# Kernel tuning notes

Hardware: AMD Instinct MI355X
Metric: run time of the kernel (lower is better)

Reference implementation:

```python
import jax, jax.numpy as jnp
import numpy as np

# Graph sizes: users -> items ('ui') and users -> tags ('ut'), plus reverse etypes.
N_U, N_I, N_T, D = 100000, 50000, 20000, 128
E_UI, E_UT = 500000, 300000


def setup_inputs() -> dict:
    key = jax.random.key(0)
    k = jax.random.split(key, 7)
    return {
        "h_u": jax.random.normal(k[0], (N_U, D), jnp.float32),
        "h_i": jax.random.normal(k[1], (N_I, D), jnp.float32),
        "h_t": jax.random.normal(k[2], (N_T, D), jnp.float32),
        "ui_src": jax.random.randint(k[3], (E_UI,), 0, N_U, jnp.int32),
        "ui_dst": jax.random.randint(k[4], (E_UI,), 0, N_I, jnp.int32),
        "ut_src": jax.random.randint(k[5], (E_UT,), 0, N_U, jnp.int32),
        "ut_dst": jax.random.randint(k[6], (E_UT,), 0, N_T, jnp.int32),
    }


def _seg_sum(x, idx, n):
    return jax.ops.segment_sum(x, idx, num_segments=n)


def _deg(idx, n):
    # in-degree, clamped to min 1 (as torch .clamp(min=1))
    return jnp.clip(_seg_sum(jnp.ones(idx.shape, jnp.float32), idx, n), 1.0, None)


def reference(h_u, h_i, h_t, ui_src, ui_dst, ut_src, ut_dst):
    NORM_2 = -1.0  # default norm_2 arg
    # forward pass: copy_u('h') + sum per etype, then 1/in_degree normalization on dst
    rst_i = _seg_sum(h_u[ui_src], ui_dst, N_I) / _deg(ui_dst, N_I)[:, None]  # [N_I, D]
    rst_t = _seg_sum(h_u[ut_src], ut_dst, N_T) / _deg(ut_dst, N_T)[:, None]  # [N_T, D]
    # backward pass: multi_update_all over reverse etypes, 'sum' cross-etype reducer
    bsrc = _seg_sum(rst_i[ui_dst], ui_src, N_U) + _seg_sum(rst_t[ut_dst], ut_src, N_U)
    # in_degrees_b: per-etype clamped degrees summed across reverse etypes
    deg_b = _deg(ui_src, N_U) + _deg(ut_src, N_U)
    bsrc = bsrc * (deg_b ** NORM_2)[:, None]
    # rst is the LAST etype's normalized dst result ('ut' -> tags)
    return bsrc, rst_t
```

## Files before the change

### kernel.cpp

```cpp
#include <hip/hip_runtime.h>

#define NU 100000
#define NI 50000
#define NT 20000
#define DD 128
#define EUI 500000
#define EUT 300000

#define B_I   0
#define B_T   (NI)
#define B_UUI (NI + NT)
#define B_UUT (NI + NT + NU)
#define NSCAN (NI + NT + NU + NU)
#define TOTAL_E (2 * (EUI + EUT))

#define BPB   512
#define NB    ((NSCAN + BPB - 1) / BPB)
#define CH    8192
#define NBLK  ((TOTAL_E + CH - 1) / CH)
#define NHIST (NB * NBLK)

__device__ __forceinline__ unsigned bfpack(float a, float b) {
    unsigned ua = __float_as_uint(a), ub = __float_as_uint(b);
    ua = (ua + 0x7FFFu + ((ua >> 16) & 1u)) >> 16;
    ub = (ub + 0x7FFFu + ((ub >> 16) & 1u)) >> 16;
    return ua | (ub << 16);
}
__device__ __forceinline__ void bacc(unsigned p, float& a, float& b) {
    a += __uint_as_float(p << 16);
    b += __uint_as_float(p & 0xFFFF0000u);
}

__device__ __forceinline__ void entry_of(int e,
        const int* __restrict__ ui_src, const int* __restrict__ ui_dst,
        const int* __restrict__ ut_src, const int* __restrict__ ut_dst,
        int& bucket, int& val) {
    if (e < EUI)              { bucket = B_I   + ui_dst[e];              val = ui_src[e]; }
    else if (e < 2 * EUI)     { int j = e - EUI;       bucket = B_UUI + ui_src[j]; val = ui_dst[j]; }
    else if (e < 2 * EUI + EUT){ int j = e - 2 * EUI;   bucket = B_T   + ut_dst[j]; val = ut_src[j]; }
    else                      { int j = e - 2 * EUI - EUT; bucket = B_UUT + ut_src[j]; val = ut_dst[j]; }
}


__global__ void k_hist(const int* __restrict__ ui_src, const int* __restrict__ ui_dst,
                       const int* __restrict__ ut_src, const int* __restrict__ ut_dst,
                       int* __restrict__ hist) {
    __shared__ int h[NB];
    int b = blockIdx.x, t = threadIdx.x;
    for (int i = t; i < NB; i += 256) h[i] = 0;
    __syncthreads();
    int e0 = b * CH;
    int e1 = min(e0 + CH, TOTAL_E);
    for (int e = e0 + t; e < e1; e += 256) {
        int bucket, val;
        entry_of(e, ui_src, ui_dst, ut_src, ut_dst, bucket, val);
        (void)val;
        atomicAdd(&h[bucket >> 9], 1);
    }
    __syncthreads();
    for (int i = t; i < NB; i += 256) hist[i * NBLK + b] = h[i];
}

__global__ void k_scanA(int* __restrict__ data, int* __restrict__ bsums, int n) {
    __shared__ int lds[256];
    int b = blockIdx.x, t = threadIdx.x;
    int base = b * 1024 + t * 4;
    int v0 = (base + 0 < n) ? data[base + 0] : 0;
    int v1 = (base + 1 < n) ? data[base + 1] : 0;
    int v2 = (base + 2 < n) ? data[base + 2] : 0;
    int v3 = (base + 3 < n) ? data[base + 3] : 0;
    int i0 = v0, i1 = i0 + v1, i2 = i1 + v2, i3 = i2 + v3;
    lds[t] = i3;
    __syncthreads();
    for (int o = 1; o < 256; o <<= 1) {
        int x = (t >= o) ? lds[t - o] : 0;
        __syncthreads();
        lds[t] += x;
        __syncthreads();
    }
    int ex = lds[t] - i3;
    if (base + 0 < n) data[base + 0] = ex + i0;
    if (base + 1 < n) data[base + 1] = ex + i1;
    if (base + 2 < n) data[base + 2] = ex + i2;
    if (base + 3 < n) data[base + 3] = ex + i3;
    if (t == 255) bsums[b] = lds[255];
}

__global__ void k_scanB(int* __restrict__ bsums, int nsb) {
    __shared__ int lds[512];
    int t = threadIdx.x;
    int a = (t < nsb) ? bsums[t] : 0;
    int b2 = (t + 256 < nsb) ? bsums[t + 256] : 0;
    lds[t] = a;
    lds[t + 256] = b2;
    __syncthreads();
    for (int o = 1; o < 512; o <<= 1) {
        int x0 = (t >= o) ? lds[t - o] : 0;
        int x1 = (t + 256 >= o) ? lds[t + 256 - o] : 0;
        __syncthreads();
        lds[t] += x0;
        lds[t + 256] += x1;
        __syncthreads();
    }
    if (t < nsb) bsums[t] = lds[t] - a;
    if (t + 256 < nsb) bsums[t + 256] = lds[t + 256] - b2;
}

__global__ void k_scanC(int* __restrict__ data, const int* __restrict__ bsums, int n) {
    int b = blockIdx.x;
    int add = bsums[b];
    int base = b * 1024 + threadIdx.x * 4;
    if (base + 0 < n) data[base + 0] += add;
    if (base + 1 < n) data[base + 1] += add;
    if (base + 2 < n) data[base + 2] += add;
    if (base + 3 < n) data[base + 3] += add;
}

__global__ void k_scatterbin(const int* __restrict__ ui_src, const int* __restrict__ ui_dst,
                             const int* __restrict__ ut_src, const int* __restrict__ ut_dst,
                             const int* __restrict__ hist, unsigned* __restrict__ binned) {
    __shared__ int loff[NB];
    int b = blockIdx.x, t = threadIdx.x;
    for (int i = t; i < NB; i += 256) loff[i] = hist[i * NBLK + b];
    __syncthreads();
    int e0 = b * CH;
    int e1 = min(e0 + CH, TOTAL_E);
    for (int e = e0 + t; e < e1; e += 256) {
        int bucket, val;
        entry_of(e, ui_src, ui_dst, ut_src, ut_dst, bucket, val);
        int bin = bucket >> 9;
        int pos = atomicAdd(&loff[bin], -1) - 1;
        binned[pos] = ((unsigned)(bucket & (BPB - 1)) << 17) | (unsigned)val;
    }
}


__global__ void k_bincount(const unsigned* __restrict__ binned,
                           const int* __restrict__ hist, int* __restrict__ off) {
    __shared__ int cnt[BPB];
    int b = blockIdx.x, t = threadIdx.x;
    cnt[t] = 0; cnt[t + 256] = 0;
    __syncthreads();
    int s = (b == 0) ? 0 : hist[b * NBLK - 1];
    int e = hist[(b + 1) * NBLK - 1];
    for (int i = s + t; i < e; i += 256) atomicAdd(&cnt[binned[i] >> 17], 1);
    __syncthreads();
    int base = b * BPB;
    if (base + t < NSCAN) off[base + t] = cnt[t];
    if (base + t + 256 < NSCAN) off[base + t + 256] = cnt[t + 256];
}

__global__ void k_finescatter(const unsigned* __restrict__ binned,
                              const int* __restrict__ hist,
                              int* __restrict__ off, int* __restrict__ edges) {
    __shared__ int loff[BPB];
    int b = blockIdx.x, t = threadIdx.x;
    int base = b * BPB;
    if (base + t < NSCAN) loff[t] = off[base + t];
    if (base + t + 256 < NSCAN) loff[t + 256] = off[base + t + 256];
    __syncthreads();
    int s = (b == 0) ? 0 : hist[b * NBLK - 1];
    int e = hist[(b + 1) * NBLK - 1];
    for (int i = s + t; i < e; i += 256) {
        unsigned v = binned[i];
        int local = v >> 17;
        int pos = atomicAdd(&loff[local], -1) - 1;
        edges[pos] = (int)(v & 0x1FFFFu);
    }
    __syncthreads();
    if (base + t < NSCAN) off[base + t] = loff[t];
    if (base + t + 256 < NSCAN) off[base + t + 256] = loff[t + 256];
}

__global__ void k_cvt(const float4* __restrict__ in, uint4* __restrict__ out) {
    int t = blockIdx.x * blockDim.x + threadIdx.x;
    if (t >= NU * DD / 8) return;
    float4 a = in[t * 2 + 0];
    float4 b = in[t * 2 + 1];
    uint4 o;
    o.x = bfpack(a.x, a.y); o.y = bfpack(a.z, a.w);
    o.z = bfpack(b.x, b.y); o.w = bfpack(b.z, b.w);
    out[t] = o;
}

__global__ void k_gather_fwd_b(const uint2* __restrict__ feat,
                               const int* __restrict__ off, const int* __restrict__ edges,
                               uint2* __restrict__ outb, float4* __restrict__ outf,
                               int base, int nrows) {
    int tid = blockIdx.x * blockDim.x + threadIdx.x;
    int r = tid >> 5;
    int c = tid & 31;
    if (r >= nrows) return;
    int g = base + r;
    int start = off[g];
    int end = (g + 1 < NSCAN) ? off[g + 1] : TOTAL_E;
    float a0 = 0.f, a1 = 0.f, a2 = 0.f, a3 = 0.f;
    float b0 = 0.f, b1 = 0.f, b2 = 0.f, b3 = 0.f;
    int e = start;
    for (; e + 2 <= end; e += 2) {
        int s0 = edges[e], s1 = edges[e + 1];
        uint2 p0 = feat[(size_t)s0 * 32 + c];
        uint2 p1 = feat[(size_t)s1 * 32 + c];
        bacc(p0.x, a0, a1); bacc(p0.y, a2, a3);
        bacc(p1.x, b0, b1); bacc(p1.y, b2, b3);
    }
    if (e < end) {
        uint2 p = feat[(size_t)edges[e] * 32 + c];
        bacc(p.x, a0, a1); bacc(p.y, a2, a3);
    }
    float inv = 1.0f / fmaxf((float)(end - start), 1.0f);
    a0 = (a0 + b0) * inv; a1 = (a1 + b1) * inv;
    a2 = (a2 + b2) * inv; a3 = (a3 + b3) * inv;
    uint2 ob; ob.x = bfpack(a0, a1); ob.y = bfpack(a2, a3);
    outb[(size_t)r * 32 + c] = ob;
    if (outf) {
        float4 of; of.x = a0; of.y = a1; of.z = a2; of.w = a3;
        outf[(size_t)r * 32 + c] = of;
    }
}

__global__ void k_gather_fwd_f(const float4* __restrict__ feat,
                               const int* __restrict__ off, const int* __restrict__ edges,
                               uint2* __restrict__ outb, float4* __restrict__ outf,
                               int base, int nrows) {
    int tid = blockIdx.x * blockDim.x + threadIdx.x;
    int r = tid >> 5;
    int c = tid & 31;
    if (r >= nrows) return;
    int g = base + r;
    int start = off[g];
    int end = (g + 1 < NSCAN) ? off[g + 1] : TOTAL_E;
    float a0 = 0.f, a1 = 0.f, a2 = 0.f, a3 = 0.f;
    float b0 = 0.f, b1 = 0.f, b2 = 0.f, b3 = 0.f;
    int e = start;
    for (; e + 2 <= end; e += 2) {
        int s0 = edges[e], s1 = edges[e + 1];
        float4 v0 = feat[(size_t)s0 * 32 + c];
        float4 v1 = feat[(size_t)s1 * 32 + c];
        a0 += v0.x; a1 += v0.y; a2 += v0.z; a3 += v0.w;
        b0 += v1.x; b1 += v1.y; b2 += v1.z; b3 += v1.w;
    }
    if (e < end) {
        float4 v = feat[(size_t)edges[e] * 32 + c];
        a0 += v.x; a1 += v.y; a2 += v.z; a3 += v.w;
    }
    float inv = 1.0f / fmaxf((float)(end - start), 1.0f);
    a0 = (a0 + b0) * inv; a1 = (a1 + b1) * inv;
    a2 = (a2 + b2) * inv; a3 = (a3 + b3) * inv;
    uint2 ob; ob.x = bfpack(a0, a1); ob.y = bfpack(a2, a3);
    outb[(size_t)r * 32 + c] = ob;
    if (outf) {
        float4 of; of.x = a0; of.y = a1; of.z = a2; of.w = a3;
        outf[(size_t)r * 32 + c] = of;
    }
}

__global__ void k_gather_bwd_b(const uint2* __restrict__ rst_i,
                               const uint2* __restrict__ rst_t,
                               const int* __restrict__ off, const int* __restrict__ edges,
                               float4* __restrict__ bsrc) {
    int tid = blockIdx.x * blockDim.x + threadIdx.x;
    int r = tid >> 5;
    int c = tid & 31;
    if (r >= NU) return;
    int g1 = B_UUI + r;
    int s1 = off[g1], e1 = off[g1 + 1];
    int g2 = B_UUT + r;
    int s2 = off[g2], e2 = (g2 + 1 < NSCAN) ? off[g2 + 1] : TOTAL_E;
    float a0 = 0.f, a1 = 0.f, a2 = 0.f, a3 = 0.f;
    float b0 = 0.f, b1 = 0.f, b2 = 0.f, b3 = 0.f;
    int e = s1;
    for (; e + 2 <= e1; e += 2) {
        int d0 = edges[e], d1 = edges[e + 1];
        uint2 p0 = rst_i[(size_t)d0 * 32 + c];
        uint2 p1 = rst_i[(size_t)d1 * 32 + c];
        bacc(p0.x, a0, a1); bacc(p0.y, a2, a3);
        bacc(p1.x, b0, b1); bacc(p1.y, b2, b3);
    }
    if (e < e1) {
        uint2 p = rst_i[(size_t)edges[e] * 32 + c];
        bacc(p.x, a0, a1); bacc(p.y, a2, a3);
    }
    e = s2;
    for (; e + 2 <= e2; e += 2) {
        int d0 = edges[e], d1 = edges[e + 1];
        uint2 p0 = rst_t[(size_t)d0 * 32 + c];
        uint2 p1 = rst_t[(size_t)d1 * 32 + c];
        bacc(p0.x, a0, a1); bacc(p0.y, a2, a3);
        bacc(p1.x, b0, b1); bacc(p1.y, b2, b3);
    }
    if (e < e2) {
        uint2 p = rst_t[(size_t)edges[e] * 32 + c];
        bacc(p.x, a0, a1); bacc(p.y, a2, a3);
    }
    float inv = 1.0f / (fmaxf((float)(e1 - s1), 1.0f) + fmaxf((float)(e2 - s2), 1.0f));
    float4 o;
    o.x = (a0 + b0) * inv; o.y = (a1 + b1) * inv;
    o.z = (a2 + b2) * inv; o.w = (a3 + b3) * inv;
    bsrc[(size_t)r * 32 + c] = o;
}

__global__ void k_count_old(const int4* __restrict__ ui_src, const int4* __restrict__ ui_dst,
                            const int4* __restrict__ ut_src, const int4* __restrict__ ut_dst,
                            int* __restrict__ off) {
    int i = blockIdx.x * blockDim.x + threadIdx.x;
    if (i < EUI / 4) {
        int4 s = ui_src[i], d = ui_dst[i];
        atomicAdd(&off[B_I + d.x], 1); atomicAdd(&off[B_I + d.y], 1);
        atomicAdd(&off[B_I + d.z], 1); atomicAdd(&off[B_I + d.w], 1);
        atomicAdd(&off[B_UUI + s.x], 1); atomicAdd(&off[B_UUI + s.y], 1);
        atomicAdd(&off[B_UUI + s.z], 1); atomicAdd(&off[B_UUI + s.w], 1);
    } else if (i < EUI / 4 + EUT / 4) {
        int j = i - EUI / 4;
        int4 s = ut_src[j], d = ut_dst[j];
        atomicAdd(&off[B_T + d.x], 1); atomicAdd(&off[B_T + d.y], 1);
        atomicAdd(&off[B_T + d.z], 1); atomicAdd(&off[B_T + d.w], 1);
        atomicAdd(&off[B_UUT + s.x], 1); atomicAdd(&off[B_UUT + s.y], 1);
        atomicAdd(&off[B_UUT + s.z], 1); atomicAdd(&off[B_UUT + s.w], 1);
    }
}

__global__ void k_fill_old(const int2* __restrict__ ui_src, const int2* __restrict__ ui_dst,
                           const int2* __restrict__ ut_src, const int2* __restrict__ ut_dst,
                           int* __restrict__ off, int* __restrict__ edges) {
    int i = blockIdx.x * blockDim.x + threadIdx.x;
    if (i < EUI / 2) {
        int2 s = ui_src[i], d = ui_dst[i];
        edges[atomicAdd(&off[B_I + d.x], -1) - 1] = s.x;
        edges[atomicAdd(&off[B_UUI + s.x], -1) - 1] = d.x;
        edges[atomicAdd(&off[B_I + d.y], -1) - 1] = s.y;
        edges[atomicAdd(&off[B_UUI + s.y], -1) - 1] = d.y;
    } else if (i < EUI / 2 + EUT / 2) {
        int j = i - EUI / 2;
        int2 s = ut_src[j], d = ut_dst[j];
        edges[atomicAdd(&off[B_T + d.x], -1) - 1] = s.x;
        edges[atomicAdd(&off[B_UUT + s.x], -1) - 1] = d.x;
        edges[atomicAdd(&off[B_T + d.y], -1) - 1] = s.y;
        edges[atomicAdd(&off[B_UUT + s.y], -1) - 1] = d.y;
    }
}

__global__ void f_count(const int* __restrict__ ui_src, const int* __restrict__ ui_dst,
                        const int* __restrict__ ut_src, const int* __restrict__ ut_dst,
                        float* __restrict__ cnt_uui, float* __restrict__ cnt_i,
                        float* __restrict__ cnt_uut, float* __restrict__ cnt_t) {
    int i = blockIdx.x * blockDim.x + threadIdx.x;
    if (i < EUI) {
        unsafeAtomicAdd(&cnt_uui[ui_src[i]], 1.0f);
        unsafeAtomicAdd(&cnt_i[ui_dst[i]], 1.0f);
    } else if (i < EUI + EUT) {
        int j = i - EUI;
        unsafeAtomicAdd(&cnt_uut[ut_src[j]], 1.0f);
        unsafeAtomicAdd(&cnt_t[ut_dst[j]], 1.0f);
    }
}
__global__ void f_scatter_fwd(const float4* __restrict__ feat, const int* __restrict__ src,
                              const int* __restrict__ dst, float* __restrict__ out_sum, int nedge) {
    int tid = blockIdx.x * blockDim.x + threadIdx.x;
    int e = tid >> 5, c = tid & 31;
    if (e >= nedge) return;
    float4 v = feat[(size_t)src[e] * 32 + c];
    float* o = out_sum + (size_t)dst[e] * DD + c * 4;
    unsafeAtomicAdd(o + 0, v.x); unsafeAtomicAdd(o + 1, v.y);
    unsafeAtomicAdd(o + 2, v.z); unsafeAtomicAdd(o + 3, v.w);
}
__global__ void f_scatter_bwd(const float4* __restrict__ rst_sum, const float* __restrict__ cnt,
                              const int* __restrict__ src, const int* __restrict__ dst,
                              float* __restrict__ bsrc, int nedge) {
    int tid = blockIdx.x * blockDim.x + threadIdx.x;
    int e = tid >> 5, c = tid & 31;
    if (e >= nedge) return;
    float inv = 1.0f / fmaxf(cnt[dst[e]], 1.0f);
    float4 v = rst_sum[(size_t)dst[e] * 32 + c];
    float* o = bsrc + (size_t)src[e] * DD + c * 4;
    unsafeAtomicAdd(o + 0, v.x * inv); unsafeAtomicAdd(o + 1, v.y * inv);
    unsafeAtomicAdd(o + 2, v.z * inv); unsafeAtomicAdd(o + 3, v.w * inv);
}
__global__ void f_norm(float4* __restrict__ rst, const float* __restrict__ cnt, int nrows) {
    int tid = blockIdx.x * blockDim.x + threadIdx.x;
    int r = tid >> 5, c = tid & 31;
    if (r >= nrows) return;
    float inv = 1.0f / fmaxf(cnt[r], 1.0f);
    float4 v = rst[(size_t)r * 32 + c];
    v.x *= inv; v.y *= inv; v.z *= inv; v.w *= inv;
    rst[(size_t)r * 32 + c] = v;
}
__global__ void f_final(float4* __restrict__ bsrc, const float* __restrict__ cnt_a,
                        const float* __restrict__ cnt_b, int nrows) {
    int tid = blockIdx.x * blockDim.x + threadIdx.x;
    int r = tid >> 5, c = tid & 31;
    if (r >= nrows) return;
    float inv = 1.0f / (fmaxf(cnt_a[r], 1.0f) + fmaxf(cnt_b[r], 1.0f));
    float4 v = bsrc[(size_t)r * 32 + c];
    v.x *= inv; v.y *= inv; v.z *= inv; v.w *= inv;
    bsrc[(size_t)r * 32 + c] = v;
}


extern "C" void kernel_launch(void* const* d_in, const int* in_sizes, int n_in,
                              void* d_out, int out_size, void* d_ws, size_t ws_size,
                              hipStream_t stream) {
    const float* h_u  = (const float*)d_in[0];
    const int* ui_src = (const int*)d_in[3];
    const int* ui_dst = (const int*)d_in[4];
    const int* ut_src = (const int*)d_in[5];
    const int* ut_dst = (const int*)d_in[6];

    float* bsrc  = (float*)d_out;
    float* rst_t = (float*)d_out + (size_t)NU * DD;

    const int B = 256;

    const size_t INT_WORDS = (size_t)NSCAN + 512 + TOTAL_E;
    const size_t BASE_B    = INT_WORDS * 4;
    const size_t HUB_B     = (size_t)NU * DD * 2;
    const size_t RIB_B     = (size_t)NI * DD * 2;
    const size_t RTB_B     = (size_t)NT * DD * 2;
    const size_t NEED_FULL = BASE_B + HUB_B + RIB_B + RTB_B;
    const size_t NEED_HALF = BASE_B + RIB_B + RTB_B;

    if (ws_size >= NEED_FULL) {
        int* off      = (int*)d_ws;
        int* bsums    = off + NSCAN;
        int* edges    = bsums + 512;
        uint2* hu_b   = (uint2*)((char*)d_ws + BASE_B);
        uint2* rsti_b = (uint2*)((char*)d_ws + BASE_B + HUB_B);
        uint2* rstt_b = (uint2*)((char*)d_ws + BASE_B + HUB_B + RIB_B);
        unsigned* binned = (unsigned*)rsti_b;
        int* hist        = (int*)rstt_b;

        k_cvt<<<(NU * DD / 8 + B - 1) / B, B, 0, stream>>>(
            (const float4*)h_u, (uint4*)hu_b);

        k_hist<<<NBLK, B, 0, stream>>>(ui_src, ui_dst, ut_src, ut_dst, hist);

        {
            int nblk = (NHIST + 1023) / 1024;
            k_scanA<<<nblk, B, 0, stream>>>(hist, bsums, NHIST);
            k_scanB<<<1, B, 0, stream>>>(bsums, nblk);
            k_scanC<<<nblk, B, 0, stream>>>(hist, bsums, NHIST);
        }

        k_scatterbin<<<NBLK, B, 0, stream>>>(ui_src, ui_dst, ut_src, ut_dst, hist, binned);

        k_bincount<<<NB, B, 0, stream>>>(binned, hist, off);

        {
            int nblk = (NSCAN + 1023) / 1024;
            k_scanA<<<nblk, B, 0, stream>>>(off, bsums, NSCAN);
            k_scanB<<<1, B, 0, stream>>>(bsums, nblk);
            k_scanC<<<nblk, B, 0, stream>>>(off, bsums, NSCAN);
        }

        k_finescatter<<<NB, B, 0, stream>>>(binned, hist, off, edges);

        k_gather_fwd_b<<<((long)NI * 32 + B - 1) / B, B, 0, stream>>>(
            hu_b, off, edges, rsti_b, (float4*)nullptr, B_I, NI);
        k_gather_fwd_b<<<((long)NT * 32 + B - 1) / B, B, 0, stream>>>(
            hu_b, off, edges, rstt_b, (float4*)rst_t, B_T, NT);
        k_gather_bwd_b<<<((long)NU * 32 + B - 1) / B, B, 0, stream>>>(
            rsti_b, rstt_b, off, edges, (float4*)bsrc);
    } else if (ws_size >= NEED_HALF) {
        int* off   = (int*)d_ws;
        int* bsums = off + NSCAN;
        int* edges = bsums + 512;
        uint2* rsti_b = (uint2*)((char*)d_ws + BASE_B);
        uint2* rstt_b = (uint2*)((char*)d_ws + BASE_B + RIB_B);

        hipMemsetAsync(off, 0, (NSCAN + 512) * sizeof(int), stream);

        int nq = EUI / 4 + EUT / 4;
        k_count_old<<<(nq + B - 1) / B, B, 0, stream>>>(
            (const int4*)ui_src, (const int4*)ui_dst,
            (const int4*)ut_src, (const int4*)ut_dst, off);
        {
            int nblk = (NSCAN + 1023) / 1024;
            k_scanA<<<nblk, B, 0, stream>>>(off, bsums, NSCAN);
            k_scanB<<<1, B, 0, stream>>>(bsums, nblk);
            k_scanC<<<nblk, B, 0, stream>>>(off, bsums, NSCAN);
        }
        int nh = EUI / 2 + EUT / 2;
        k_fill_old<<<(nh + B - 1) / B, B, 0, stream>>>(
            (const int2*)ui_src, (const int2*)ui_dst,
            (const int2*)ut_src, (const int2*)ut_dst, off, edges);

        k_gather_fwd_f<<<((long)NI * 32 + B - 1) / B, B, 0, stream>>>(
            (const float4*)h_u, off, edges, rsti_b, (float4*)nullptr, B_I, NI);
        k_gather_fwd_f<<<((long)NT * 32 + B - 1) / B, B, 0, stream>>>(
            (const float4*)h_u, off, edges, rstt_b, (float4*)rst_t, B_T, NT);
        k_gather_bwd_b<<<((long)NU * 32 + B - 1) / B, B, 0, stream>>>(
            rsti_b, rstt_b, off, edges, (float4*)bsrc);
    } else {
        float* ws        = (float*)d_ws;
        float* rst_i_sum = ws;
        float* cnt_i     = rst_i_sum + (size_t)NI * DD;
        float* cnt_t     = cnt_i + NI;
        float* cnt_uui   = cnt_t + NT;
        float* cnt_uut   = cnt_uui + NU;
        size_t ws_floats = (size_t)NI * DD + NI + NT + NU + NU;

        hipMemsetAsync(d_ws, 0, ws_floats * sizeof(float), stream);
        hipMemsetAsync(d_out, 0, (size_t)out_size * sizeof(float), stream);

        int n = EUI + EUT;
        f_count<<<(n + B - 1) / B, B, 0, stream>>>(ui_src, ui_dst, ut_src, ut_dst,
                                                   cnt_uui, cnt_i, cnt_uut, cnt_t);
        f_scatter_fwd<<<((long)EUI * 32 + B - 1) / B, B, 0, stream>>>(
            (const float4*)h_u, ui_src, ui_dst, rst_i_sum, EUI);
        f_scatter_fwd<<<((long)EUT * 32 + B - 1) / B, B, 0, stream>>>(
            (const float4*)h_u, ut_src, ut_dst, rst_t, EUT);
        f_scatter_bwd<<<((long)EUI * 32 + B - 1) / B, B, 0, stream>>>(
            (const float4*)rst_i_sum, cnt_i, ui_src, ui_dst, bsrc, EUI);
        f_scatter_bwd<<<((long)EUT * 32 + B - 1) / B, B, 0, stream>>>(
            (const float4*)rst_t, cnt_t, ut_src, ut_dst, bsrc, EUT);
        f_norm<<<((long)NT * 32 + B - 1) / B, B, 0, stream>>>((float4*)rst_t, cnt_t, NT);
        f_final<<<((long)NU * 32 + B - 1) / B, B, 0, stream>>>((float4*)bsrc, cnt_uui, cnt_uut, NU);
    }
}
```

Before: 194.5 us.

## Merge forward gathers and use 16-lane rows with uint4 loads and shuffled indices

Replaces the two forward gather launches with one kernel covering item and tag rows, since their CSR offsets are contiguous. Both forward and backward gathers now assign 16 lanes per row, with each lane loading 8 bf16 values as a uint4. Each lane loads one edge index per batch of 16, and the index is broadcast with a width-16 shuffle instead of every lane reading it. The aim is fewer launches, wider memory transactions and less index traffic. The cost is the loss of the dual-accumulator unrolling and more register pressure per thread. The old 32-lane kernels are kept, simplified, for the fallback path.

```diff
diff --git a/kernel.cpp b/kernel.cpp
--- a/kernel.cpp
+++ b/kernel.cpp
@@ -40,7 +40,6 @@
     else if (e < 2 * EUI + EUT){ int j = e - 2 * EUI;   bucket = B_T   + ut_dst[j]; val = ut_src[j]; }
     else                      { int j = e - 2 * EUI - EUT; bucket = B_UUT + ut_src[j]; val = ut_dst[j]; }
 }
-
 
 __global__ void k_hist(const int* __restrict__ ui_src, const int* __restrict__ ui_dst,
                        const int* __restrict__ ut_src, const int* __restrict__ ut_dst,
@@ -134,7 +133,6 @@
     }
 }
 
-
 __global__ void k_bincount(const unsigned* __restrict__ binned,
                            const int* __restrict__ hist, int* __restrict__ off) {
     __shared__ int cnt[BPB];
@@ -183,121 +181,84 @@
     out[t] = o;
 }
 
-__global__ void k_gather_fwd_b(const uint2* __restrict__ feat,
-                               const int* __restrict__ off, const int* __restrict__ edges,
-                               uint2* __restrict__ outb, float4* __restrict__ outf,
-                               int base, int nrows) {
-    int tid = blockIdx.x * blockDim.x + threadIdx.x;
-    int r = tid >> 5;
-    int c = tid & 31;
-    if (r >= nrows) return;
-    int g = base + r;
-    int start = off[g];
-    int end = (g + 1 < NSCAN) ? off[g + 1] : TOTAL_E;
-    float a0 = 0.f, a1 = 0.f, a2 = 0.f, a3 = 0.f;
-    float b0 = 0.f, b1 = 0.f, b2 = 0.f, b3 = 0.f;
-    int e = start;
-    for (; e + 2 <= end; e += 2) {
-        int s0 = edges[e], s1 = edges[e + 1];
-        uint2 p0 = feat[(size_t)s0 * 32 + c];
-        uint2 p1 = feat[(size_t)s1 * 32 + c];
-        bacc(p0.x, a0, a1); bacc(p0.y, a2, a3);
-        bacc(p1.x, b0, b1); bacc(p1.y, b2, b3);
-    }
-    if (e < end) {
-        uint2 p = feat[(size_t)edges[e] * 32 + c];
-        bacc(p.x, a0, a1); bacc(p.y, a2, a3);
+
+__global__ void g_fwd(const uint4* __restrict__ feat,
+                      const int* __restrict__ off, const int* __restrict__ edges,
+                      uint4* __restrict__ rsti_b, uint4* __restrict__ rstt_b,
+                      float4* __restrict__ outf) {
+    int tid = blockIdx.x * blockDim.x + threadIdx.x;
+    int r = tid >> 4;
+    int c = tid & 15;
+    if (r >= NI + NT) return;
+    int start = off[r];
+    int end = off[r + 1];
+    float a0=0.f,a1=0.f,a2=0.f,a3=0.f,a4=0.f,a5=0.f,a6=0.f,a7=0.f;
+    for (int base = start; base < end; base += 16) {
+        int n = min(16, end - base);
+        int eidx = (c < n) ? edges[base + c] : 0;
+        #pragma unroll 4
+        for (int k = 0; k < n; ++k) {
+            int s = __shfl(eidx, k, 16);
+            uint4 p = feat[(size_t)s * 16 + c];
+            bacc(p.x, a0, a1); bacc(p.y, a2, a3);
+            bacc(p.z, a4, a5); bacc(p.w, a6, a7);
+        }
     }
     float inv = 1.0f / fmaxf((float)(end - start), 1.0f);
-    a0 = (a0 + b0) * inv; a1 = (a1 + b1) * inv;
-    a2 = (a2 + b2) * inv; a3 = (a3 + b3) * inv;
-    uint2 ob; ob.x = bfpack(a0, a1); ob.y = bfpack(a2, a3);
-    outb[(size_t)r * 32 + c] = ob;
-    if (outf) {
-        float4 of; of.x = a0; of.y = a1; of.z = a2; of.w = a3;
-        outf[(size_t)r * 32 + c] = of;
-    }
-}
-
-__global__ void k_gather_fwd_f(const float4* __restrict__ feat,
-                               const int* __restrict__ off, const int* __restrict__ edges,
-                               uint2* __restrict__ outb, float4* __restrict__ outf,
-                               int base, int nrows) {
-    int tid = blockIdx.x * blockDim.x + threadIdx.x;
-    int r = tid >> 5;
-    int c = tid & 31;
-    if (r >= nrows) return;
-    int g = base + r;
-    int start = off[g];
-    int end = (g + 1 < NSCAN) ? off[g + 1] : TOTAL_E;
-    float a0 = 0.f, a1 = 0.f, a2 = 0.f, a3 = 0.f;
-    float b0 = 0.f, b1 = 0.f, b2 = 0.f, b3 = 0.f;
-    int e = start;
-    for (; e + 2 <= end; e += 2) {
-        int s0 = edges[e], s1 = edges[e + 1];
-        float4 v0 = feat[(size_t)s0 * 32 + c];
-        float4 v1 = feat[(size_t)s1 * 32 + c];
-        a0 += v0.x; a1 += v0.y; a2 += v0.z; a3 += v0.w;
-        b0 += v1.x; b1 += v1.y; b2 += v1.z; b3 += v1.w;
-    }
-    if (e < end) {
-        float4 v = feat[(size_t)edges[e] * 32 + c];
-        a0 += v.x; a1 += v.y; a2 += v.z; a3 += v.w;
-    }
-    float inv = 1.0f / fmaxf((float)(end - start), 1.0f);
-    a0 = (a0 + b0) * inv; a1 = (a1 + b1) * inv;
-    a2 = (a2 + b2) * inv; a3 = (a3 + b3) * inv;
-    uint2 ob; ob.x = bfpack(a0, a1); ob.y = bfpack(a2, a3);
-    outb[(size_t)r * 32 + c] = ob;
-    if (outf) {
-        float4 of; of.x = a0; of.y = a1; of.z = a2; of.w = a3;
-        outf[(size_t)r * 32 + c] = of;
-    }
-}
-
-__global__ void k_gather_bwd_b(const uint2* __restrict__ rst_i,
-                               const uint2* __restrict__ rst_t,
-                               const int* __restrict__ off, const int* __restrict__ edges,
-                               float4* __restrict__ bsrc) {
-    int tid = blockIdx.x * blockDim.x + threadIdx.x;
-    int r = tid >> 5;
-    int c = tid & 31;
+    a0*=inv; a1*=inv; a2*=inv; a3*=inv; a4*=inv; a5*=inv; a6*=inv; a7*=inv;
+    uint4 ob;
+    ob.x = bfpack(a0,a1); ob.y = bfpack(a2,a3);
+    ob.z = bfpack(a4,a5); ob.w = bfpack(a6,a7);
+    if (r < NI) {
+        rsti_b[(size_t)r * 16 + c] = ob;
+    } else {
+        int rt = r - NI;
+        rstt_b[(size_t)rt * 16 + c] = ob;
+        float4 f0; f0.x=a0; f0.y=a1; f0.z=a2; f0.w=a3;
+        float4 f1; f1.x=a4; f1.y=a5; f1.z=a6; f1.w=a7;
+        outf[(size_t)rt * 32 + c*2 + 0] = f0;
+        outf[(size_t)rt * 32 + c*2 + 1] = f1;
+    }
+}
+
+__global__ void g_bwd(const uint4* __restrict__ rst_i, const uint4* __restrict__ rst_t,
+                      const int* __restrict__ off, const int* __restrict__ edges,
+                      float4* __restrict__ bsrc) {
+    int tid = blockIdx.x * blockDim.x + threadIdx.x;
+    int r = tid >> 4;
+    int c = tid & 15;
     if (r >= NU) return;
-    int g1 = B_UUI + r;
-    int s1 = off[g1], e1 = off[g1 + 1];
+    int s1 = off[B_UUI + r], e1 = off[B_UUI + r + 1];
     int g2 = B_UUT + r;
     int s2 = off[g2], e2 = (g2 + 1 < NSCAN) ? off[g2 + 1] : TOTAL_E;
-    float a0 = 0.f, a1 = 0.f, a2 = 0.f, a3 = 0.f;
-    float b0 = 0.f, b1 = 0.f, b2 = 0.f, b3 = 0.f;
-    int e = s1;
-    for (; e + 2 <= e1; e += 2) {
-        int d0 = edges[e], d1 = edges[e + 1];
-        uint2 p0 = rst_i[(size_t)d0 * 32 + c];
-        uint2 p1 = rst_i[(size_t)d1 * 32 + c];
-        bacc(p0.x, a0, a1); bacc(p0.y, a2, a3);
-        bacc(p1.x, b0, b1); bacc(p1.y, b2, b3);
-    }
-    if (e < e1) {
-        uint2 p = rst_i[(size_t)edges[e] * 32 + c];
-        bacc(p.x, a0, a1); bacc(p.y, a2, a3);
-    }
-    e = s2;
-    for (; e + 2 <= e2; e += 2) {
-        int d0 = edges[e], d1 = edges[e + 1];
-        uint2 p0 = rst_t[(size_t)d0 * 32 + c];
-        uint2 p1 = rst_t[(size_t)d1 * 32 + c];
-        bacc(p0.x, a0, a1); bacc(p0.y, a2, a3);
-        bacc(p1.x, b0, b1); bacc(p1.y, b2, b3);
-    }
-    if (e < e2) {
-        uint2 p = rst_t[(size_t)edges[e] * 32 + c];
-        bacc(p.x, a0, a1); bacc(p.y, a2, a3);
+    float a0=0.f,a1=0.f,a2=0.f,a3=0.f,a4=0.f,a5=0.f,a6=0.f,a7=0.f;
+    for (int base = s1; base < e1; base += 16) {
+        int n = min(16, e1 - base);
+        int eidx = (c < n) ? edges[base + c] : 0;
+        #pragma unroll 4
+        for (int k = 0; k < n; ++k) {
+            int d = __shfl(eidx, k, 16);
+            uint4 p = rst_i[(size_t)d * 16 + c];
+            bacc(p.x, a0, a1); bacc(p.y, a2, a3);
+            bacc(p.z, a4, a5); bacc(p.w, a6, a7);
+        }
+    }
+    for (int base = s2; base < e2; base += 16) {
+        int n = min(16, e2 - base);
+        int eidx = (c < n) ? edges[base + c] : 0;
+        #pragma unroll 4
+        for (int k = 0; k < n; ++k) {
+            int d = __shfl(eidx, k, 16);
+            uint4 p = rst_t[(size_t)d * 16 + c];
+            bacc(p.x, a0, a1); bacc(p.y, a2, a3);
+            bacc(p.z, a4, a5); bacc(p.w, a6, a7);
+        }
     }
     float inv = 1.0f / (fmaxf((float)(e1 - s1), 1.0f) + fmaxf((float)(e2 - s2), 1.0f));
-    float4 o;
-    o.x = (a0 + b0) * inv; o.y = (a1 + b1) * inv;
-    o.z = (a2 + b2) * inv; o.w = (a3 + b3) * inv;
-    bsrc[(size_t)r * 32 + c] = o;
+    float4 f0; f0.x=a0*inv; f0.y=a1*inv; f0.z=a2*inv; f0.w=a3*inv;
+    float4 f1; f1.x=a4*inv; f1.y=a5*inv; f1.z=a6*inv; f1.w=a7*inv;
+    bsrc[(size_t)r * 32 + c*2 + 0] = f0;
+    bsrc[(size_t)r * 32 + c*2 + 1] = f1;
 }
 
 __global__ void k_count_old(const int4* __restrict__ ui_src, const int4* __restrict__ ui_dst,
@@ -340,6 +301,59 @@
     }
 }
 
+__global__ void k_gather_fwd_f(const float4* __restrict__ feat,
+                               const int* __restrict__ off, const int* __restrict__ edges,
+                               uint2* __restrict__ outb, float4* __restrict__ outf,
+                               int base, int nrows) {
+    int tid = blockIdx.x * blockDim.x + threadIdx.x;
+    int r = tid >> 5;
+    int c = tid & 31;
+    if (r >= nrows) return;
+    int g = base + r;
+    int start = off[g];
+    int end = (g + 1 < NSCAN) ? off[g + 1] : TOTAL_E;
+    float a0 = 0.f, a1 = 0.f, a2 = 0.f, a3 = 0.f;
+    for (int e = start; e < end; ++e) {
+        float4 v = feat[(size_t)edges[e] * 32 + c];
+        a0 += v.x; a1 += v.y; a2 += v.z; a3 += v.w;
+    }
+    float inv = 1.0f / fmaxf((float)(end - start), 1.0f);
+    a0 *= inv; a1 *= inv; a2 *= inv; a3 *= inv;
+    uint2 ob; ob.x = bfpack(a0, a1); ob.y = bfpack(a2, a3);
+    outb[(size_t)r * 32 + c] = ob;
+    if (outf) {
+        float4 of; of.x = a0; of.y = a1; of.z = a2; of.w = a3;
+        outf[(size_t)r * 32 + c] = of;
+    }
+}
+
+__global__ void k_gather_bwd_b(const uint2* __restrict__ rst_i,
+                               const uint2* __restrict__ rst_t,
+                               const int* __restrict__ off, const int* __restrict__ edges,
+                               float4* __restrict__ bsrc) {
+    int tid = blockIdx.x * blockDim.x + threadIdx.x;
+    int r = tid >> 5;
+    int c = tid & 31;
+    if (r >= NU) return;
+    int g1 = B_UUI + r;
+    int s1 = off[g1], e1 = off[g1 + 1];
+    int g2 = B_UUT + r;
+    int s2 = off[g2], e2 = (g2 + 1 < NSCAN) ? off[g2 + 1] : TOTAL_E;
+    float a0 = 0.f, a1 = 0.f, a2 = 0.f, a3 = 0.f;
+    for (int e = s1; e < e1; ++e) {
+        uint2 p = rst_i[(size_t)edges[e] * 32 + c];
+        bacc(p.x, a0, a1); bacc(p.y, a2, a3);
+    }
+    for (int e = s2; e < e2; ++e) {
+        uint2 p = rst_t[(size_t)edges[e] * 32 + c];
+        bacc(p.x, a0, a1); bacc(p.y, a2, a3);
+    }
+    float inv = 1.0f / (fmaxf((float)(e1 - s1), 1.0f) + fmaxf((float)(e2 - s2), 1.0f));
+    float4 o;
+    o.x = a0 * inv; o.y = a1 * inv; o.z = a2 * inv; o.w = a3 * inv;
+    bsrc[(size_t)r * 32 + c] = o;
+}
+
 __global__ void f_count(const int* __restrict__ ui_src, const int* __restrict__ ui_dst,
                         const int* __restrict__ ut_src, const int* __restrict__ ut_dst,
                         float* __restrict__ cnt_uui, float* __restrict__ cnt_i,
@@ -423,14 +437,14 @@
         int* off      = (int*)d_ws;
         int* bsums    = off + NSCAN;
         int* edges    = bsums + 512;
-        uint2* hu_b   = (uint2*)((char*)d_ws + BASE_B);
-        uint2* rsti_b = (uint2*)((char*)d_ws + BASE_B + HUB_B);
-        uint2* rstt_b = (uint2*)((char*)d_ws + BASE_B + HUB_B + RIB_B);
+        uint4* hu_b   = (uint4*)((char*)d_ws + BASE_B);
+        uint4* rsti_b = (uint4*)((char*)d_ws + BASE_B + HUB_B);
+        uint4* rstt_b = (uint4*)((char*)d_ws + BASE_B + HUB_B + RIB_B);
         unsigned* binned = (unsigned*)rsti_b;
         int* hist        = (int*)rstt_b;
 
         k_cvt<<<(NU * DD / 8 + B - 1) / B, B, 0, stream>>>(
-            (const float4*)h_u, (uint4*)hu_b);
+            (const float4*)h_u, hu_b);
 
         k_hist<<<NBLK, B, 0, stream>>>(ui_src, ui_dst, ut_src, ut_dst, hist);
 
@@ -454,11 +468,9 @@
 
         k_finescatter<<<NB, B, 0, stream>>>(binned, hist, off, edges);
 
-        k_gather_fwd_b<<<((long)NI * 32 + B - 1) / B, B, 0, stream>>>(
-            hu_b, off, edges, rsti_b, (float4*)nullptr, B_I, NI);
-        k_gather_fwd_b<<<((long)NT * 32 + B - 1) / B, B, 0, stream>>>(
-            hu_b, off, edges, rstt_b, (float4*)rst_t, B_T, NT);
-        k_gather_bwd_b<<<((long)NU * 32 + B - 1) / B, B, 0, stream>>>(
+        g_fwd<<<((long)(NI + NT) * 16 + B - 1) / B, B, 0, stream>>>(
+            hu_b, off, edges, rsti_b, rstt_b, (float4*)rst_t);
+        g_bwd<<<((long)NU * 16 + B - 1) / B, B, 0, stream>>>(
             rsti_b, rstt_b, off, edges, (float4*)bsrc);
     } else if (ws_size >= NEED_HALF) {
         int* off   = (int*)d_ws;
```

After: 182.7 us. -6.1%, faster.
